# Kernel tuning notes

Hardware: AMD Instinct MI355X
Metric: run time of the kernel (lower is better)

## Reference

```python
import jax, jax.numpy as jnp
import numpy as np

B, N, C, G, H, DK = 8, 128, 128, 2, 4, 32
BN_SCALE = float(1.0 / np.sqrt(1.0 + 1e-5))  # eval-mode BatchNorm with running_mean=0, var=1, gamma=1, beta=0


def _l1norm(x):
    # F.normalize(p=1, dim=-1)
    return x / jnp.maximum(jnp.sum(jnp.abs(x), -1, keepdims=True), 1e-12)


def _bn(x):
    return x * BN_SCALE


def _lrelu(x):
    return jax.nn.leaky_relu(x, 0.01)


def setup_inputs() -> dict:
    key = jax.random.key(0)
    ks = jax.random.split(key, 14)
    p = lambda i, shape: jax.random.normal(ks[i], shape, jnp.float32) * 0.05
    return {
        "vp": jax.random.normal(ks[0], (B, N, C), jnp.float32),
        "ep0": jax.random.uniform(ks[1], (B, N, N), jnp.float32),
        # PointSimilarity_Pre 1x1-conv stack (stored as [in, out] matrices)
        "ps_pre_w1": p(2, (C, 2 * C)), "ps_pre_w2": p(3, (2 * C, C)),
        "ps_pre_w3": p(4, (C, 1)), "ps_pre_b3": jnp.zeros((1,), jnp.float32),
        # Per-generation PointSimilarity2 stacks
        "ps_w1": p(5, (G, C, 2 * C)), "ps_w2": p(6, (G, 2 * C, C)),
        "ps_w3": p(7, (G, C, 1)), "ps_b3": jnp.zeros((G, 1), jnp.float32),
        # Per-generation D2PAgg stacks (input is cat(vp, aggr) -> 2C channels)
        "d2p_w1": p(8, (G, 2 * C, 2 * C)), "d2p_w2": p(9, (G, 2 * C, C)),
        # Per-generation multi-head attention projections (d_model=C, n_head*d_k=C)
        "mha_wq": p(10, (G, C, H * DK)), "mha_wk": p(11, (G, C, H * DK)),
    }


def _psim(vp, ep_last, w1, w2, w3, b3, kval):
    # pairwise l2 distance features: [B, N, N, C]
    sim = (vp[:, :, None, :] - vp[:, None, :, :]) ** 2
    h = _lrelu(_bn(jnp.einsum('bijc,co->bijo', sim, w1)))
    h = _lrelu(_bn(jnp.einsum('bijc,co->bijo', h, w2)))
    e = jax.nn.sigmoid(jnp.einsum('bijc,co->bijo', h, w3)[..., 0] + b3)
    eye = jnp.eye(vp.shape[1], dtype=vp.dtype)
    ep_last = ep_last * (1.0 - eye)
    ep_sum = jnp.sum(ep_last, -1, keepdims=True)
    e = e * ep_last
    if kval is not None:  # neighbor attention via top-k sparsification
        _, idx = jax.lax.top_k(e, kval)
        b_i = jnp.arange(e.shape[0])[:, None, None]
        r_i = jnp.arange(e.shape[1])[None, :, None]
        mask = jnp.zeros_like(e).at[b_i, r_i, idx].set(1.0)
        e = e * mask
    e = _l1norm(e) * ep_sum
    e = e + eye + 1e-6
    e = e / jnp.sum(e, 2, keepdims=True)
    return e


def _d2p(ep, vp, w1, w2):
    eye = jnp.eye(vp.shape[1], dtype=vp.dtype)
    edge = _l1norm(ep * (1.0 - eye))
    aggr = jnp.einsum('bij,bjc->bic', edge, vp)  # bmm aggregation
    nf = jnp.concatenate([vp, aggr], -1)         # [B, N, 2C]
    h = _lrelu(_bn(nf @ w1))
    return _lrelu(_bn(h @ w2))


def _mha(vp, wq, wk):
    b, n, _ = vp.shape
    q = (vp @ wq).reshape(b, n, H, DK)
    k = (vp @ wk).reshape(b, n, H, DK)
    attn = jax.nn.softmax(jnp.einsum('bqhd,bkhd->bhqk', q, k) / np.sqrt(DK), axis=-1)
    return attn.mean(1)  # average heads -> [B, N, N]


def reference(vp, ep0, ps_pre_w1, ps_pre_w2, ps_pre_w3, ps_pre_b3,
              ps_w1, ps_w2, ps_w3, ps_b3, d2p_w1, d2p_w2, mha_wq, mha_wk):
    ep = _psim(vp, ep0, ps_pre_w1, ps_pre_w2, ps_pre_w3, ps_pre_b3, None)
    for g in range(G):
        attn = _mha(vp, mha_wq[g], mha_wk[g])
        vp = _d2p(ep * attn, vp, d2p_w1[g], d2p_w2[g])
        kval = int(N * (1.0 - 0.1 * (g + 1)))
        ep = _psim(vp, ep, ps_w1[g], ps_w2[g], ps_w3[g], ps_b3[g], kval)
    return ep
```

## Files before the change

kernel.cpp:

```cpp
#include <hip/hip_runtime.h>

typedef __bf16 bf16x8 __attribute__((ext_vector_type(8)));
typedef float floatx4 __attribute__((ext_vector_type(4)));

#define MFMA(a, b, c) __builtin_amdgcn_mfma_f32_16x16x32_bf16(a, b, c, 0, 0, 0)

#define BNS 0.9999950000374997f
#define LRELU(x) ((x) > 0.f ? (x) : 0.01f * (x))

__device__ inline float wave_sum(float v) {
#pragma unroll
  for (int s = 32; s > 0; s >>= 1) v += __shfl_xor(v, s, 64);
  return v;
}
__device__ inline float wave_max(float v) {
#pragma unroll
  for (int s = 32; s > 0; s >>= 1) v = fmaxf(v, __shfl_xor(v, s, 64));
  return v;
}

__global__ __launch_bounds__(256) void k_prep(const float* __restrict__ pre_w1,
                                              const float* __restrict__ ps_w1,
                                              const float* __restrict__ pre_w2,
                                              const float* __restrict__ ps_w2,
                                              __bf16* __restrict__ w1b,
                                              __bf16* __restrict__ w2b) {
  const int tt = blockIdx.x * 256 + threadIdx.x;
  const int buf = tt / 12288;
  const int r = tt % 12288;
  const int set = r >> 12;
  const int q = r & 4095;
  const int ln = q & 63, qd = ln >> 4, cc = ln & 15;
  const int wv = (q >> 6) & 3;
  bf16x8 v;
  if (buf == 0) {
    const int kt = (q >> 8) & 3, qtr = (q >> 10) & 3;
    const float* src = (set == 0) ? pre_w1 : ps_w1 + (size_t)(set - 1) * 32768;
    const float* p = src + (size_t)(kt * 32 + qd * 8) * 256 + qtr * 64 + wv * 16 + cc;
#pragma unroll
    for (int jj = 0; jj < 8; jj++) v[jj] = (__bf16)p[jj * 256];
    *(bf16x8*)&w1b[(size_t)set * 32768 + q * 8] = v;
  } else {
    const int kt = (q >> 8) & 1, nt = (q >> 9) & 1, qtr = (q >> 10) & 3;
    const float* src = (set == 0) ? pre_w2 : ps_w2 + (size_t)(set - 1) * 32768;
    const float* p = src + (size_t)(qtr * 64 + kt * 32 + qd * 8) * 128 + wv * 32 + nt * 16 + cc;
#pragma unroll
    for (int jj = 0; jj < 8; jj++) v[jj] = (__bf16)p[jj * 128];
    *(bf16x8*)&w2b[(size_t)set * 32768 + q * 8] = v;
  }
}

__global__ void __launch_bounds__(256, 3)
k_psim(const float* __restrict__ vp, const float* __restrict__ ep_in,
       float* __restrict__ ep_out,
       const __bf16* __restrict__ w1b, const __bf16* __restrict__ w2b,
       const float* __restrict__ w3, const float* __restrict__ b3,
       int kval, float* __restrict__ outp) {
  __shared__ __bf16 simf[16384];
  __shared__ __bf16 hbf[8192];
  __shared__ float ep_row[128];
  __shared__ float e_row[128];
  __shared__ float w3s[128];
  __shared__ float red[256];
  __shared__ float red2[4];

  const int tid = threadIdx.x;
  const int b = blockIdx.x >> 7, i = blockIdx.x & 127;
  const float* vpb = vp + ((size_t)b << 14);
  const float* vpi = vpb + (i << 7);
  const size_t rowoff = ((size_t)blockIdx.x) << 7;

  {
    const int j = tid >> 1;
    const int c0 = (tid & 1) << 6;
    const int m = j >> 4, ccr = j & 15;
    const float* vpj = vpb + (j << 7) + c0;
    const float* vpx = vpi + c0;
#pragma unroll
    for (int c = 0; c < 64; c += 8) {
      const int gc = c0 + c;
      const int kt = gc >> 5, qdw = (gc >> 3) & 3;
      float4 a0 = *(const float4*)(vpj + c);
      float4 a1 = *(const float4*)(vpj + c + 4);
      float4 b0 = *(const float4*)(vpx + c);
      float4 b1 = *(const float4*)(vpx + c + 4);
      bf16x8 t;
      float d;
      d = a0.x - b0.x; t[0] = (__bf16)(d * d);
      d = a0.y - b0.y; t[1] = (__bf16)(d * d);
      d = a0.z - b0.z; t[2] = (__bf16)(d * d);
      d = a0.w - b0.w; t[3] = (__bf16)(d * d);
      d = a1.x - b1.x; t[4] = (__bf16)(d * d);
      d = a1.y - b1.y; t[5] = (__bf16)(d * d);
      d = a1.z - b1.z; t[6] = (__bf16)(d * d);
      d = a1.w - b1.w; t[7] = (__bf16)(d * d);
      *(bf16x8*)&simf[(((kt << 3) + m) << 6 | (qdw << 4 | ccr)) << 3] = t;
    }
    if (tid < 128) {
      ep_row[tid] = (tid == i) ? 0.f : ep_in[rowoff + tid];
      w3s[tid] = w3[tid];
    }
  }
  __syncthreads();

  const int wv = tid >> 6;
  const int ln = tid & 63;
  const int qd = ln >> 4;
  const int cc = ln & 15;

  floatx4 acc2[8][2];
#pragma unroll
  for (int m = 0; m < 8; m++) {
    acc2[m][0] = (floatx4){0.f, 0.f, 0.f, 0.f};
    acc2[m][1] = (floatx4){0.f, 0.f, 0.f, 0.f};
  }

  const int h1h = wv >> 1;
  const int h1qd = ((wv & 1) << 1) | (cc >> 3);
  const int h1jj = cc & 7;

  for (int qtr = 0; qtr < 4; qtr++) {
    bf16x8 bw[4];
#pragma unroll
    for (int kt = 0; kt < 4; kt++)
      bw[kt] = *(const bf16x8*)&w1b[((((qtr * 4 + kt) * 4 + wv) * 64) + ln) * 8];
#pragma unroll
    for (int m2 = 0; m2 < 8; m2 += 2) {
      bf16x8 af0[4], af1[4];
#pragma unroll
      for (int kt = 0; kt < 4; kt++) {
        af0[kt] = *(const bf16x8*)&simf[(((kt << 3) + m2) << 6 | ln) << 3];
        af1[kt] = *(const bf16x8*)&simf[(((kt << 3) + m2 + 1) << 6 | ln) << 3];
      }
      floatx4 x0 = (floatx4){0.f, 0.f, 0.f, 0.f};
      floatx4 x1 = (floatx4){0.f, 0.f, 0.f, 0.f};
#pragma unroll
      for (int kt = 0; kt < 4; kt++) {
        x0 = MFMA(af0[kt], bw[kt], x0);
        x1 = MFMA(af1[kt], bw[kt], x1);
      }
#pragma unroll
      for (int r = 0; r < 4; r++) {
        float v0 = x0[r] * BNS;
        float v1 = x1[r] * BNS;
        hbf[(((h1h * 8 + m2) * 64) + h1qd * 16 + qd * 4 + r) * 8 + h1jj] = (__bf16)LRELU(v0);
        hbf[(((h1h * 8 + m2 + 1) * 64) + h1qd * 16 + qd * 4 + r) * 8 + h1jj] = (__bf16)LRELU(v1);
      }
    }
    __syncthreads();

    bf16x8 bw2[2][2];
#pragma unroll
    for (int nt = 0; nt < 2; nt++)
#pragma unroll
      for (int kt = 0; kt < 2; kt++)
        bw2[nt][kt] = *(const bf16x8*)&w2b[(((((qtr * 2 + nt) * 2 + kt) * 4 + wv) * 64) + ln) * 8];
#pragma unroll
    for (int m = 0; m < 8; m++) {
      bf16x8 a0 = *(const bf16x8*)&hbf[((m << 6) | ln) << 3];
      bf16x8 a1 = *(const bf16x8*)&hbf[(((8 + m) << 6) | ln) << 3];
      acc2[m][0] = MFMA(a0, bw2[0][0], acc2[m][0]);
      acc2[m][1] = MFMA(a0, bw2[1][0], acc2[m][1]);
      acc2[m][0] = MFMA(a1, bw2[0][1], acc2[m][0]);
      acc2[m][1] = MFMA(a1, bw2[1][1], acc2[m][1]);
    }
    __syncthreads();
  }

  {
    const int seg = wv;
#pragma unroll
    for (int m = 0; m < 8; m++)
#pragma unroll
      for (int nt = 0; nt < 2; nt++) {
        const int q2 = (nt << 1) | (cc >> 3);
#pragma unroll
        for (int r = 0; r < 4; r++) {
          float v = acc2[m][nt][r] * BNS;
          simf[(((seg * 8 + m) * 64) + q2 * 16 + qd * 4 + r) * 8 + (cc & 7)] = (__bf16)LRELU(v);
        }
      }
  }
  __syncthreads();

  {
    const int j = tid & 127, hh = tid >> 7;
    const int m = j >> 4, R = j & 15;
    float s = 0.f;
#pragma unroll
    for (int sg = 0; sg < 2; sg++) {
      const int seg = hh * 2 + sg;
#pragma unroll
      for (int q3 = 0; q3 < 4; q3++) {
        bf16x8 f = *(const bf16x8*)&simf[(((seg * 8 + m) * 64) + q3 * 16 + R) * 8];
        const float* wp = &w3s[seg * 32 + q3 * 8];
#pragma unroll
        for (int jj = 0; jj < 8; jj++) s += (float)f[jj] * wp[jj];
      }
    }
    red[tid] = s;
  }
  __syncthreads();
  if (tid < 128) {
    float s = red[tid] + red[tid + 128] + b3[0];
    float sg = 1.f / (1.f + expf(-s));
    e_row[tid] = sg * ep_row[tid];
  }
  __syncthreads();

  {
    float v = (tid < 128) ? ep_row[tid] : 0.f;
    float w = wave_sum(v);
    if (ln == 0) red2[wv] = w;
  }
  __syncthreads();
  const float ep_sum = red2[0] + red2[1];

  if (kval > 0) {
    const int j = tid & 127, hh = tid >> 7;
    const float v = e_row[j];
    int cnt = 0;
    const int base = hh << 6;
#pragma unroll 8
    for (int jj = 0; jj < 64; jj++) {
      float u = e_row[base + jj];
      cnt += (u > v || (u == v && (base + jj) < j)) ? 1 : 0;
    }
    red[tid] = (float)cnt;
  }
  __syncthreads();

  float em = 0.f;
  if (tid < 128) {
    float v = e_row[tid];
    if (kval > 0) {
      int cnt = (int)red[tid] + (int)red[tid + 128];
      em = (cnt < kval) ? v : 0.f;
    } else {
      em = v;
    }
  }
  {
    float w = wave_sum((tid < 128) ? em : 0.f);
    if (ln == 0) red2[wv] = w;
  }
  __syncthreads();
  const float l1 = red2[0] + red2[1];
  __syncthreads();

  const float scale = ep_sum / fmaxf(l1, 1e-12f);
  float val = 0.f;
  if (tid < 128) val = em * scale + ((tid == i) ? 1.f : 0.f) + 1e-6f;
  {
    float w = wave_sum((tid < 128) ? val : 0.f);
    if (ln == 0) red2[wv] = w;
  }
  __syncthreads();
  const float rsum = red2[0] + red2[1];

  if (tid < 128) {
    float o = val / rsum;
    ep_out[rowoff + tid] = o;
    if (outp) outp[rowoff + tid] = o;
  }
}

__global__ __launch_bounds__(256) void k_qk(const float* __restrict__ vp,
                                            const float* __restrict__ wq,
                                            const float* __restrict__ wk,
                                            float* __restrict__ qo,
                                            float* __restrict__ ko) {
  __shared__ float vr[128];
  const int t = threadIdx.x;
  const size_t rowoff = ((size_t)blockIdx.x) << 7;
  if (t < 128) vr[t] = vp[rowoff + t];
  __syncthreads();
  const int o = t & 127;
  const float* w = (t < 128) ? wq : wk;
  float a = 0.f;
#pragma unroll 8
  for (int c = 0; c < 128; c++) a += vr[c] * w[c * 128 + o];
  float* dst = (t < 128) ? qo : ko;
  dst[rowoff + o] = a;
}

__global__ __launch_bounds__(256) void k_attn_d2p(const float* __restrict__ qv,
                                                  const float* __restrict__ kv,
                                                  const float* __restrict__ ep,
                                                  const float* __restrict__ vp_in,
                                                  const float* __restrict__ w1,
                                                  const float* __restrict__ w2,
                                                  float* __restrict__ vp_out) {
  __shared__ float qi[128];
  __shared__ float sbuf[512];
  __shared__ float er[128];
  __shared__ float nf[256];
  __shared__ float hb[256];
  __shared__ float red2[4];

  const int tid = threadIdx.x;
  const int wv = tid >> 6, ln = tid & 63;
  const int j = tid & 127, hh = tid >> 7;
  const int b = blockIdx.x >> 7, i = blockIdx.x & 127;
  const size_t rowoff = ((size_t)blockIdx.x) << 7;
  const float* vpbb = vp_in + ((size_t)b << 14);

  if (tid < 128) qi[tid] = qv[rowoff + tid];
  __syncthreads();

  {
    const float* krow = kv + (((size_t)(b * 128 + j)) << 7);
    const int h0 = hh * 2, h1 = hh * 2 + 1;
    float s0 = 0.f, s1 = 0.f;
#pragma unroll
    for (int d = 0; d < 32; d += 4) {
      float4 k0 = *(const float4*)(krow + h0 * 32 + d);
      float4 k1 = *(const float4*)(krow + h1 * 32 + d);
      s0 += qi[h0 * 32 + d] * k0.x + qi[h0 * 32 + d + 1] * k0.y +
            qi[h0 * 32 + d + 2] * k0.z + qi[h0 * 32 + d + 3] * k0.w;
      s1 += qi[h1 * 32 + d] * k1.x + qi[h1 * 32 + d + 1] * k1.y +
            qi[h1 * 32 + d + 2] * k1.z + qi[h1 * 32 + d + 3] * k1.w;
    }
    sbuf[h0 * 128 + j] = s0 * 0.17677669529663687f;
    sbuf[h1 * 128 + j] = s1 * 0.17677669529663687f;
  }
  __syncthreads();

  {
    const int g = tid >> 6;
    float a = sbuf[g * 128 + ln];
    float bv = sbuf[g * 128 + ln + 64];
    float mx = wave_max(fmaxf(a, bv));
    float e0 = expf(a - mx), e1 = expf(bv - mx);
    float Z = wave_sum(e0 + e1);
    sbuf[g * 128 + ln] = e0 / Z;
    sbuf[g * 128 + ln + 64] = e1 / Z;
  }
  __syncthreads();

  float eraw = 0.f;
  if (tid < 128) {
    float attn = 0.25f * (sbuf[j] + sbuf[128 + j] + sbuf[256 + j] + sbuf[384 + j]);
    eraw = (j == i) ? 0.f : ep[rowoff + j] * attn;
  }
  {
    float w = wave_sum((tid < 128) ? eraw : 0.f);
    if (ln == 0) red2[wv] = w;
  }
  __syncthreads();
  const float l1 = red2[0] + red2[1];
  if (tid < 128) {
    er[j] = eraw / fmaxf(l1, 1e-12f);
    nf[j] = vp_in[rowoff + j];
  }
  __syncthreads();

  if (tid >= 128) {
    const int c = tid - 128;
    float a = 0.f;
#pragma unroll 8
    for (int jj = 0; jj < 128; jj++) a += er[jj] * vpbb[(jj << 7) + c];
    nf[128 + c] = a;
  }
  __syncthreads();
  {
    float hv = 0.f;
#pragma unroll 8
    for (int c2 = 0; c2 < 256; c2++) hv += nf[c2] * w1[c2 * 256 + tid];
    hv *= BNS;
    hb[tid] = LRELU(hv);
  }
  __syncthreads();
  if (tid < 128) {
    float ov = 0.f;
#pragma unroll 8
    for (int o = 0; o < 256; o++) ov += hb[o] * w2[o * 128 + tid];
    ov *= BNS;
    vp_out[rowoff + tid] = LRELU(ov);
  }
}

extern "C" void kernel_launch(void* const* d_in, const int* in_sizes, int n_in,
                              void* d_out, int out_size, void* d_ws, size_t ws_size,
                              hipStream_t stream) {
  const float* vp0    = (const float*)d_in[0];
  const float* ep0    = (const float*)d_in[1];
  const float* pre_w1 = (const float*)d_in[2];
  const float* pre_w2 = (const float*)d_in[3];
  const float* pre_w3 = (const float*)d_in[4];
  const float* pre_b3 = (const float*)d_in[5];
  const float* ps_w1  = (const float*)d_in[6];
  const float* ps_w2  = (const float*)d_in[7];
  const float* ps_w3  = (const float*)d_in[8];
  const float* ps_b3  = (const float*)d_in[9];
  const float* dw1    = (const float*)d_in[10];
  const float* dw2    = (const float*)d_in[11];
  const float* mwq    = (const float*)d_in[12];
  const float* mwk    = (const float*)d_in[13];

  char* ws = (char*)d_ws;
  float* ep   = (float*)(ws);
  float* vpb  = (float*)(ws + (512ull << 10));
  float* vpa  = (float*)(ws + (1024ull << 10));
  float* qf   = (float*)(ws + (1536ull << 10));
  float* kf   = (float*)(ws + (2048ull << 10));
  __bf16* w1b = (__bf16*)(ws + (2560ull << 10));
  __bf16* w2b = (__bf16*)(ws + (2560ull << 10) + 196608);
  float* outp = (float*)d_out;

  k_prep<<<96, 256, 0, stream>>>(pre_w1, ps_w1, pre_w2, ps_w2, w1b, w2b);

  k_psim<<<1024, 256, 0, stream>>>(vp0, ep0, ep, w1b, w2b, pre_w3, pre_b3, 0, nullptr);

  k_qk<<<1024, 256, 0, stream>>>(vp0, mwq, mwk, qf, kf);
  k_attn_d2p<<<1024, 256, 0, stream>>>(qf, kf, ep, vp0, dw1, dw2, vpb);
  k_psim<<<1024, 256, 0, stream>>>(vpb, ep, ep, w1b + 32768, w2b + 32768,
                                   ps_w3, ps_b3, 115, nullptr);

  k_qk<<<1024, 256, 0, stream>>>(vpb, mwq + 16384, mwk + 16384, qf, kf);
  k_attn_d2p<<<1024, 256, 0, stream>>>(qf, kf, ep, vpb, dw1 + 65536, dw2 + 32768, vpa);
  k_psim<<<1024, 256, 0, stream>>>(vpa, ep, ep, w1b + 65536, w2b + 65536,
                                   ps_w3 + 128, ps_b3 + 1, 102, outp);
}
```

Before: 268.7 us.

## Process two rows per attn_d2p block and use packed bf16 weights for small GEMVs

The prep kernel now also converts the D2P and Q/K projection weights to bf16, interleaved so each thread loads 8 consecutive input channels with one vector load. k_attn_d2p handles two query rows per block, which halves the grid and reuses every weight and key load across both rows. Its aggregation step is split across all threads with float4 loads and a partial-sum reduction in shared memory. The aim is to cut global weight traffic in these GEMV-like kernels, at the cost of bf16 rounding of weights and more shared memory per block.

```diff
diff --git a/kernel.cpp b/kernel.cpp
--- a/kernel.cpp
+++ b/kernel.cpp
@@ -23,30 +23,61 @@
                                               const float* __restrict__ ps_w1,
                                               const float* __restrict__ pre_w2,
                                               const float* __restrict__ ps_w2,
+                                              const float* __restrict__ dw1,
+                                              const float* __restrict__ dw2,
+                                              const float* __restrict__ mwq,
+                                              const float* __restrict__ mwk,
                                               __bf16* __restrict__ w1b,
-                                              __bf16* __restrict__ w2b) {
+                                              __bf16* __restrict__ w2b,
+                                              __bf16* __restrict__ d1i,
+                                              __bf16* __restrict__ d2i,
+                                              __bf16* __restrict__ qki) {
   const int tt = blockIdx.x * 256 + threadIdx.x;
-  const int buf = tt / 12288;
-  const int r = tt % 12288;
-  const int set = r >> 12;
-  const int q = r & 4095;
-  const int ln = q & 63, qd = ln >> 4, cc = ln & 15;
-  const int wv = (q >> 6) & 3;
   bf16x8 v;
-  if (buf == 0) {
-    const int kt = (q >> 8) & 3, qtr = (q >> 10) & 3;
-    const float* src = (set == 0) ? pre_w1 : ps_w1 + (size_t)(set - 1) * 32768;
-    const float* p = src + (size_t)(kt * 32 + qd * 8) * 256 + qtr * 64 + wv * 16 + cc;
-#pragma unroll
-    for (int jj = 0; jj < 8; jj++) v[jj] = (__bf16)p[jj * 256];
-    *(bf16x8*)&w1b[(size_t)set * 32768 + q * 8] = v;
-  } else {
-    const int kt = (q >> 8) & 1, nt = (q >> 9) & 1, qtr = (q >> 10) & 3;
-    const float* src = (set == 0) ? pre_w2 : ps_w2 + (size_t)(set - 1) * 32768;
-    const float* p = src + (size_t)(qtr * 64 + kt * 32 + qd * 8) * 128 + wv * 32 + nt * 16 + cc;
-#pragma unroll
-    for (int jj = 0; jj < 8; jj++) v[jj] = (__bf16)p[jj * 128];
-    *(bf16x8*)&w2b[(size_t)set * 32768 + q * 8] = v;
+  if (tt < 24576) {
+    const int buf = tt / 12288;
+    const int r = tt % 12288;
+    const int set = r >> 12;
+    const int q = r & 4095;
+    const int ln = q & 63, qd = ln >> 4, cc = ln & 15;
+    const int wv = (q >> 6) & 3;
+    if (buf == 0) {
+      const int kt = (q >> 8) & 3, qtr = (q >> 10) & 3;
+      const float* src = (set == 0) ? pre_w1 : ps_w1 + (size_t)(set - 1) * 32768;
+      const float* p = src + (size_t)(kt * 32 + qd * 8) * 256 + qtr * 64 + wv * 16 + cc;
+#pragma unroll
+      for (int jj = 0; jj < 8; jj++) v[jj] = (__bf16)p[jj * 256];
+      *(bf16x8*)&w1b[(size_t)set * 32768 + q * 8] = v;
+    } else {
+      const int kt = (q >> 8) & 1, nt = (q >> 9) & 1, qtr = (q >> 10) & 3;
+      const float* src = (set == 0) ? pre_w2 : ps_w2 + (size_t)(set - 1) * 32768;
+      const float* p = src + (size_t)(qtr * 64 + kt * 32 + qd * 8) * 128 + wv * 32 + nt * 16 + cc;
+#pragma unroll
+      for (int jj = 0; jj < 8; jj++) v[jj] = (__bf16)p[jj * 128];
+      *(bf16x8*)&w2b[(size_t)set * 32768 + q * 8] = v;
+    }
+  } else if (tt < 40960) {
+    const int u = tt - 24576;
+    const int gen = u >> 13, r = u & 8191, cb = r >> 8, o = r & 255;
+    const float* src = dw1 + (size_t)gen * 65536 + (size_t)(cb * 8) * 256 + o;
+#pragma unroll
+    for (int jj = 0; jj < 8; jj++) v[jj] = (__bf16)src[jj * 256];
+    *(bf16x8*)&d1i[(size_t)(((gen * 32 + cb) * 256 + o)) * 8] = v;
+  } else if (tt < 49152) {
+    const int u = tt - 40960;
+    const int gen = u >> 12, r = u & 4095, kb = r >> 7, o = r & 127;
+    const float* src = dw2 + (size_t)gen * 32768 + (size_t)(kb * 8) * 128 + o;
+#pragma unroll
+    for (int jj = 0; jj < 8; jj++) v[jj] = (__bf16)src[jj * 128];
+    *(bf16x8*)&d2i[(size_t)(((gen * 32 + kb) * 128 + o)) * 8] = v;
+  } else if (tt < 57344) {
+    const int u = tt - 49152;
+    const int gen = u >> 12, r = u & 4095, qk = r >> 11, r2 = r & 2047;
+    const int cb = r2 >> 7, o = r2 & 127;
+    const float* src = (qk ? mwk : mwq) + (size_t)gen * 16384 + (size_t)(cb * 8) * 128 + o;
+#pragma unroll
+    for (int jj = 0; jj < 8; jj++) v[jj] = (__bf16)src[jj * 128];
+    *(bf16x8*)&qki[(size_t)((((gen * 2 + qk) * 16 + cb) * 128 + o)) * 8] = v;
   }
 }
 
@@ -266,8 +297,7 @@
 }
 
 __global__ __launch_bounds__(256) void k_qk(const float* __restrict__ vp,
-                                            const float* __restrict__ wq,
-                                            const float* __restrict__ wk,
+                                            const __bf16* __restrict__ qkw,
                                             float* __restrict__ qo,
                                             float* __restrict__ ko) {
   __shared__ float vr[128];
@@ -276,10 +306,16 @@
   if (t < 128) vr[t] = vp[rowoff + t];
   __syncthreads();
   const int o = t & 127;
-  const float* w = (t < 128) ? wq : wk;
+  const __bf16* base = qkw + ((t >> 7) ? 16384 : 0);
+  const float4* vr4 = (const float4*)vr;
   float a = 0.f;
-#pragma unroll 8
-  for (int c = 0; c < 128; c++) a += vr[c] * w[c * 128 + o];
+#pragma unroll
+  for (int cb = 0; cb < 16; cb++) {
+    bf16x8 w8 = *(const bf16x8*)&base[(cb * 128 + o) * 8];
+    float4 v0 = vr4[2 * cb], v1 = vr4[2 * cb + 1];
+    a += v0.x * (float)w8[0] + v0.y * (float)w8[1] + v0.z * (float)w8[2] + v0.w * (float)w8[3] +
+         v1.x * (float)w8[4] + v1.y * (float)w8[5] + v1.z * (float)w8[6] + v1.w * (float)w8[7];
+  }
   float* dst = (t < 128) ? qo : ko;
   dst[rowoff + o] = a;
 }
@@ -288,95 +324,137 @@
                                                   const float* __restrict__ kv,
                                                   const float* __restrict__ ep,
                                                   const float* __restrict__ vp_in,
-                                                  const float* __restrict__ w1,
-                                                  const float* __restrict__ w2,
+                                                  const __bf16* __restrict__ d1,
+                                                  const __bf16* __restrict__ d2,
                                                   float* __restrict__ vp_out) {
-  __shared__ float qi[128];
-  __shared__ float sbuf[512];
-  __shared__ float er[128];
-  __shared__ float nf[256];
-  __shared__ float hb[256];
+  __shared__ float qi[256];
+  __shared__ float sbuf[1024];
+  __shared__ float er[256];
+  __shared__ float nf[512];
+  __shared__ float hb[512];
+  __shared__ float pbuf[2048];
   __shared__ float red2[4];
 
   const int tid = threadIdx.x;
   const int wv = tid >> 6, ln = tid & 63;
-  const int j = tid & 127, hh = tid >> 7;
-  const int b = blockIdx.x >> 7, i = blockIdx.x & 127;
-  const size_t rowoff = ((size_t)blockIdx.x) << 7;
+  const int b = blockIdx.x >> 6;
+  const int r0 = (blockIdx.x & 63) * 2;
+  const size_t rowoff0 = ((size_t)(b * 128 + r0)) << 7;
   const float* vpbb = vp_in + ((size_t)b << 14);
 
-  if (tid < 128) qi[tid] = qv[rowoff + tid];
-  __syncthreads();
-
-  {
+  qi[tid] = qv[rowoff0 + tid];
+  __syncthreads();
+
+  {
+    const int j = tid & 127, hh = tid >> 7;
     const float* krow = kv + (((size_t)(b * 128 + j)) << 7);
     const int h0 = hh * 2, h1 = hh * 2 + 1;
-    float s0 = 0.f, s1 = 0.f;
+    float s00 = 0.f, s01 = 0.f, s10 = 0.f, s11 = 0.f;
 #pragma unroll
     for (int d = 0; d < 32; d += 4) {
       float4 k0 = *(const float4*)(krow + h0 * 32 + d);
       float4 k1 = *(const float4*)(krow + h1 * 32 + d);
-      s0 += qi[h0 * 32 + d] * k0.x + qi[h0 * 32 + d + 1] * k0.y +
-            qi[h0 * 32 + d + 2] * k0.z + qi[h0 * 32 + d + 3] * k0.w;
-      s1 += qi[h1 * 32 + d] * k1.x + qi[h1 * 32 + d + 1] * k1.y +
-            qi[h1 * 32 + d + 2] * k1.z + qi[h1 * 32 + d + 3] * k1.w;
-    }
-    sbuf[h0 * 128 + j] = s0 * 0.17677669529663687f;
-    sbuf[h1 * 128 + j] = s1 * 0.17677669529663687f;
-  }
-  __syncthreads();
-
-  {
-    const int g = tid >> 6;
-    float a = sbuf[g * 128 + ln];
-    float bv = sbuf[g * 128 + ln + 64];
-    float mx = wave_max(fmaxf(a, bv));
-    float e0 = expf(a - mx), e1 = expf(bv - mx);
-    float Z = wave_sum(e0 + e1);
-    sbuf[g * 128 + ln] = e0 / Z;
-    sbuf[g * 128 + ln + 64] = e1 / Z;
-  }
-  __syncthreads();
-
-  float eraw = 0.f;
-  if (tid < 128) {
-    float attn = 0.25f * (sbuf[j] + sbuf[128 + j] + sbuf[256 + j] + sbuf[384 + j]);
-    eraw = (j == i) ? 0.f : ep[rowoff + j] * attn;
-  }
-  {
-    float w = wave_sum((tid < 128) ? eraw : 0.f);
+      s00 += qi[h0 * 32 + d] * k0.x + qi[h0 * 32 + d + 1] * k0.y +
+             qi[h0 * 32 + d + 2] * k0.z + qi[h0 * 32 + d + 3] * k0.w;
+      s01 += qi[h1 * 32 + d] * k1.x + qi[h1 * 32 + d + 1] * k1.y +
+             qi[h1 * 32 + d + 2] * k1.z + qi[h1 * 32 + d + 3] * k1.w;
+      s10 += qi[128 + h0 * 32 + d] * k0.x + qi[128 + h0 * 32 + d + 1] * k0.y +
+             qi[128 + h0 * 32 + d + 2] * k0.z + qi[128 + h0 * 32 + d + 3] * k0.w;
+      s11 += qi[128 + h1 * 32 + d] * k1.x + qi[128 + h1 * 32 + d + 1] * k1.y +
+             qi[128 + h1 * 32 + d + 2] * k1.z + qi[128 + h1 * 32 + d + 3] * k1.w;
+    }
+    const float sc = 0.17677669529663687f;
+    sbuf[(0 * 4 + h0) * 128 + j] = s00 * sc;
+    sbuf[(0 * 4 + h1) * 128 + j] = s01 * sc;
+    sbuf[(1 * 4 + h0) * 128 + j] = s10 * sc;
+    sbuf[(1 * 4 + h1) * 128 + j] = s11 * sc;
+  }
+  __syncthreads();
+
+  {
+    const int g = wv;
+#pragma unroll
+    for (int row = 0; row < 2; row++) {
+      float a = sbuf[(row * 4 + g) * 128 + ln];
+      float bb = sbuf[(row * 4 + g) * 128 + 64 + ln];
+      float mx = wave_max(fmaxf(a, bb));
+      float e0 = expf(a - mx), e1 = expf(bb - mx);
+      float Z = wave_sum(e0 + e1);
+      sbuf[(row * 4 + g) * 128 + ln] = e0 / Z;
+      sbuf[(row * 4 + g) * 128 + 64 + ln] = e1 / Z;
+    }
+  }
+  __syncthreads();
+
+  {
+    const int row = tid >> 7, j = tid & 127;
+    float attn = 0.25f * (sbuf[(row * 4) * 128 + j] + sbuf[(row * 4 + 1) * 128 + j] +
+                          sbuf[(row * 4 + 2) * 128 + j] + sbuf[(row * 4 + 3) * 128 + j]);
+    float eraw = (j == r0 + row) ? 0.f : ep[rowoff0 + tid] * attn;
+    float w = wave_sum(eraw);
     if (ln == 0) red2[wv] = w;
-  }
-  __syncthreads();
-  const float l1 = red2[0] + red2[1];
-  if (tid < 128) {
-    er[j] = eraw / fmaxf(l1, 1e-12f);
-    nf[j] = vp_in[rowoff + j];
-  }
-  __syncthreads();
-
-  if (tid >= 128) {
-    const int c = tid - 128;
+    __syncthreads();
+    float l1row = red2[row * 2] + red2[row * 2 + 1];
+    er[tid] = eraw / fmaxf(l1row, 1e-12f);
+    nf[(row << 8) + j] = vp_in[rowoff0 + tid];
+  }
+  __syncthreads();
+
+  {
+    const int cg = tid & 31, jg = tid >> 5;
+    float4 a0 = {0.f, 0.f, 0.f, 0.f}, a1 = {0.f, 0.f, 0.f, 0.f};
+#pragma unroll
+    for (int jj = 0; jj < 16; jj++) {
+      const int j = jg * 16 + jj;
+      float4 v = *(const float4*)(vpbb + (j << 7) + (cg << 2));
+      float e0 = er[j], e1 = er[128 + j];
+      a0.x += e0 * v.x; a0.y += e0 * v.y; a0.z += e0 * v.z; a0.w += e0 * v.w;
+      a1.x += e1 * v.x; a1.y += e1 * v.y; a1.z += e1 * v.z; a1.w += e1 * v.w;
+    }
+    *(float4*)&pbuf[(jg * 32 + cg) * 4] = a0;
+    *(float4*)&pbuf[1024 + (jg * 32 + cg) * 4] = a1;
+  }
+  __syncthreads();
+  {
+    const int row = tid >> 7, c = tid & 127;
+    float s = 0.f;
+#pragma unroll
+    for (int jg = 0; jg < 8; jg++) s += pbuf[(row << 10) + jg * 128 + c];
+    nf[(row << 8) + 128 + c] = s;
+  }
+  __syncthreads();
+
+  {
+    const int row = tid >> 7, o = tid & 127;
+    const float4* nfr4 = (const float4*)&nf[row << 8];
+    float a0 = 0.f, a1 = 0.f;
+#pragma unroll 4
+    for (int cb = 0; cb < 32; cb++) {
+      bf16x8 wa = *(const bf16x8*)&d1[(cb * 256 + o) * 8];
+      bf16x8 wb = *(const bf16x8*)&d1[(cb * 256 + o + 128) * 8];
+      float4 n0 = nfr4[2 * cb], n1 = nfr4[2 * cb + 1];
+      a0 += n0.x * (float)wa[0] + n0.y * (float)wa[1] + n0.z * (float)wa[2] + n0.w * (float)wa[3] +
+            n1.x * (float)wa[4] + n1.y * (float)wa[5] + n1.z * (float)wa[6] + n1.w * (float)wa[7];
+      a1 += n0.x * (float)wb[0] + n0.y * (float)wb[1] + n0.z * (float)wb[2] + n0.w * (float)wb[3] +
+            n1.x * (float)wb[4] + n1.y * (float)wb[5] + n1.z * (float)wb[6] + n1.w * (float)wb[7];
+    }
+    hb[(row << 8) + o] = LRELU(a0 * BNS);
+    hb[(row << 8) + o + 128] = LRELU(a1 * BNS);
+  }
+  __syncthreads();
+
+  {
+    const int row = tid >> 7, o = tid & 127;
+    const float4* hbr4 = (const float4*)&hb[row << 8];
     float a = 0.f;
-#pragma unroll 8
-    for (int jj = 0; jj < 128; jj++) a += er[jj] * vpbb[(jj << 7) + c];
-    nf[128 + c] = a;
-  }
-  __syncthreads();
-  {
-    float hv = 0.f;
-#pragma unroll 8
-    for (int c2 = 0; c2 < 256; c2++) hv += nf[c2] * w1[c2 * 256 + tid];
-    hv *= BNS;
-    hb[tid] = LRELU(hv);
-  }
-  __syncthreads();
-  if (tid < 128) {
-    float ov = 0.f;
-#pragma unroll 8
-    for (int o = 0; o < 256; o++) ov += hb[o] * w2[o * 128 + tid];
-    ov *= BNS;
-    vp_out[rowoff + tid] = LRELU(ov);
+#pragma unroll 4
+    for (int kb = 0; kb < 32; kb++) {
+      bf16x8 w8 = *(const bf16x8*)&d2[(kb * 128 + o) * 8];
+      float4 h0 = hbr4[2 * kb], h1 = hbr4[2 * kb + 1];
+      a += h0.x * (float)w8[0] + h0.y * (float)w8[1] + h0.z * (float)w8[2] + h0.w * (float)w8[3] +
+           h1.x * (float)w8[4] + h1.y * (float)w8[5] + h1.z * (float)w8[6] + h1.w * (float)w8[7];
+    }
+    vp_out[rowoff0 + tid] = LRELU(a * BNS);
   }
 }
 
@@ -406,19 +484,23 @@
   float* kf   = (float*)(ws + (2048ull << 10));
   __bf16* w1b = (__bf16*)(ws + (2560ull << 10));
   __bf16* w2b = (__bf16*)(ws + (2560ull << 10) + 196608);
+  __bf16* d1i = (__bf16*)(ws + (2560ull << 10) + 393216);
+  __bf16* d2i = (__bf16*)(ws + (2560ull << 10) + 655360);
+  __bf16* qki = (__bf16*)(ws + (2560ull << 10) + 786432);
   float* outp = (float*)d_out;
 
-  k_prep<<<96, 256, 0, stream>>>(pre_w1, ps_w1, pre_w2, ps_w2, w1b, w2b);
+  k_prep<<<224, 256, 0, stream>>>(pre_w1, ps_w1, pre_w2, ps_w2, dw1, dw2, mwq, mwk,
+                                  w1b, w2b, d1i, d2i, qki);
 
   k_psim<<<1024, 256, 0, stream>>>(vp0, ep0, ep, w1b, w2b, pre_w3, pre_b3, 0, nullptr);
 
-  k_qk<<<1024, 256, 0, stream>>>(vp0, mwq, mwk, qf, kf);
-  k_attn_d2p<<<1024, 256, 0, stream>>>(qf, kf, ep, vp0, dw1, dw2, vpb);
+  k_qk<<<1024, 256, 0, stream>>>(vp0, qki, qf, kf);
+  k_attn_d2p<<<512, 256, 0, stream>>>(qf, kf, ep, vp0, d1i, d2i, vpb);
   k_psim<<<1024, 256, 0, stream>>>(vpb, ep, ep, w1b + 32768, w2b + 32768,
                                    ps_w3, ps_b3, 115, nullptr);
 
-  k_qk<<<1024, 256, 0, stream>>>(vpb, mwq + 16384, mwk + 16384, qf, kf);
-  k_attn_d2p<<<1024, 256, 0, stream>>>(qf, kf, ep, vpb, dw1 + 65536, dw2 + 32768, vpa);
+  k_qk<<<1024, 256, 0, stream>>>(vpb, qki + 32768, qf, kf);
+  k_attn_d2p<<<512, 256, 0, stream>>>(qf, kf, ep, vpb, d1i + 65536, d2i + 32768, vpa);
   k_psim<<<1024, 256, 0, stream>>>(vpa, ep, ep, w1b + 65536, w2b + 65536,
                                    ps_w3 + 128, ps_b3 + 1, 102, outp);
 }
```

After: 231.3 us. -13.9%, faster.
